# Kernel tuning notes

Hardware: AMD Instinct MI355X
Metric: run time of the kernel (lower is better)

## Reference

```python
import jax, jax.numpy as jnp
import numpy as np

DIM = 1024
NUM_HEADS = 16
HEAD_DIM = 64

def setup_inputs() -> dict:
    key = jax.random.key(0)
    ks = jax.random.split(key, 7)
    x = jax.random.normal(ks[0], (4, 4096, DIM), dtype=jnp.float32)
    mask = jnp.ones((4, 4096), dtype=jnp.float32)
    # torch Linear stores weight (out, in) and computes x @ W.T; we store (in, out) directly.
    Wq = jax.random.normal(ks[1], (DIM, NUM_HEADS * HEAD_DIM), dtype=jnp.float32) / np.sqrt(DIM)
    Wk = jax.random.normal(ks[2], (DIM, NUM_HEADS * HEAD_DIM), dtype=jnp.float32) / np.sqrt(DIM)
    Wv = jax.random.normal(ks[3], (DIM, NUM_HEADS * HEAD_DIM), dtype=jnp.float32) / np.sqrt(DIM)
    Wo = jax.random.normal(ks[4], (NUM_HEADS * HEAD_DIM, DIM), dtype=jnp.float32) / np.sqrt(NUM_HEADS * HEAD_DIM)
    # FeatureMap buffer: randn(dim, dim) / sqrt(dim) with dim = head_dim
    proj = jax.random.normal(ks[5], (HEAD_DIM, HEAD_DIM), dtype=jnp.float32) / np.sqrt(HEAD_DIM)
    return {"x": x, "mask": mask, "Wq": Wq, "Wk": Wk, "Wv": Wv, "Wo": Wo, "proj": proj}

def _feature_map(x, proj):
    # phi(x) = elu(x @ proj) + 1  (non-negative random features)
    return jax.nn.elu(x @ proj) + 1.0

def reference(x, mask, Wq, Wk, Wv, Wo, proj):
    b, n, _ = x.shape
    h, d = NUM_HEADS, HEAD_DIM
    # project and split heads: (b, h, n, d)
    q = (x @ Wq).reshape(b, n, h, d).transpose(0, 2, 1, 3)
    k = (x @ Wk).reshape(b, n, h, d).transpose(0, 2, 1, 3)
    v = (x @ Wv).reshape(b, n, h, d).transpose(0, 2, 1, 3)
    q = _feature_map(q, proj)
    k = _feature_map(k, proj)
    # mask: (b, n) -> (b, 1, n, 1)
    k = k * mask[:, None, :, None]
    # linear attention: phi(Q) (phi(K)^T V)
    kv = jnp.einsum('bhnd,bhne->bhde', k, v)          # (b, h, d, d)
    qkv = jnp.einsum('bhnd,bhde->bhne', q, kv)        # (b, h, n, d)
    k_sum = k.sum(axis=2)                              # (b, h, d)
    normalizer = jnp.einsum('bhnd,bhd->bhn', q, k_sum) + 1e-06
    out = qkv / normalizer[..., None]
    out = out.transpose(0, 2, 1, 3).reshape(b, n, h * d)
    return out @ Wo
```

## Files before the change

kernel.cpp:

```cpp
#include <hip/hip_runtime.h>
#include <stdint.h>

#define TOKENS 16384
#define KDIM 1024
#define QKVN 3072

typedef unsigned short u16;
using bf16x8 = __attribute__((ext_vector_type(8))) __bf16;
using f32x4  = __attribute__((ext_vector_type(4))) float;
using u16x8  = __attribute__((ext_vector_type(8))) unsigned short;

__device__ inline u16 f2bf(float f) {
  union { float f; uint32_t u; } v; v.f = f;
  uint32_t u = v.u;
  return (u16)((u + 0x7FFFu + ((u >> 16) & 1u)) >> 16);
}
__device__ inline float bf2f(u16 s) {
  union { uint32_t u; float f; } v; v.u = ((uint32_t)s) << 16;
  return v.f;
}
__device__ inline void g2l16(const void* g, void* l) {
  __builtin_amdgcn_global_load_lds(
      (const __attribute__((address_space(1))) void*)g,
      (__attribute__((address_space(3))) void*)l, 16, 0, 0);
}

template<int LD>
__device__ inline void stage_half(const u16* __restrict__ g, u16* l, int t) {
  #pragma unroll
  for (int i = 0; i < 2; ++i) {
    const int ch = i * 512 + t;
    const int row = ch >> 3;
    const int cc = (ch & 7) ^ (row & 7);
    g2l16(g + (long)row * LD + cc * 8, (char*)l + ch * 16);
  }
}

#define LDA_H(DST, BASE) do { \
  _Pragma("unroll") \
  for (int mi = 0; mi < 4; ++mi) { \
    const int row = wm*64 + mi*16 + rl; \
    const char* p = (const char*)(BASE) + row*128; \
    const int sw = (row & 7) << 4; \
    DST[mi][0] = *(const bf16x8*)(p + ((kg*16) ^ sw)); \
    DST[mi][1] = *(const bf16x8*)(p + ((64 + kg*16) ^ sw)); \
  } \
} while (0)

#define LDB_H(DST, BASE) do { \
  _Pragma("unroll") \
  for (int ni = 0; ni < 2; ++ni) { \
    const int row = wn*32 + ni*16 + rl; \
    const char* p = (const char*)(BASE) + row*128; \
    const int sw = (row & 7) << 4; \
    DST[ni][0] = *(const bf16x8*)(p + ((kg*16) ^ sw)); \
    DST[ni][1] = *(const bf16x8*)(p + ((64 + kg*16) ^ sw)); \
  } \
} while (0)

#define MFMAQ(MH, NH, AV, BV) do { \
  __builtin_amdgcn_s_setprio(1); \
  _Pragma("unroll") \
  for (int kh = 0; kh < 2; ++kh) \
    _Pragma("unroll") \
    for (int mi = 0; mi < 4; ++mi) \
      _Pragma("unroll") \
      for (int ni = 0; ni < 2; ++ni) \
        acc[(MH)*4+mi][(NH)*2+ni] = __builtin_amdgcn_mfma_f32_16x16x32_bf16( \
            AV[mi][kh], BV[ni][kh], acc[(MH)*4+mi][(NH)*2+ni], 0, 0, 0); \
  __builtin_amdgcn_s_setprio(0); \
} while (0)

#define LGKM0 do { \
  asm volatile("s_waitcnt lgkmcnt(0)" ::: "memory"); \
  __builtin_amdgcn_sched_barrier(0); \
} while (0)
#define LGKM_PRE(N) asm volatile("s_waitcnt lgkmcnt(" #N ")" ::: "memory")
#define VMC(N) asm volatile("s_waitcnt vmcnt(" #N ")" ::: "memory")
#define BAR() __builtin_amdgcn_s_barrier()

template<int NTOT, int EPI, int ALD, int NT, int PERB>
__global__ __launch_bounds__(512, 2) void gemm256(
    const u16* __restrict__ A, const u16* __restrict__ Bm,
    void* __restrict__ C, const float* __restrict__ aux) {
  __shared__ u16 As[2][2][8192];
  __shared__ u16 Bs[2][2][8192];
  const int t = threadIdx.x;
  const int l = t & 63;
  const int w = t >> 6;
  const int rl = l & 15, kg = l >> 4;
  const int wm = w >> 2, wn = w & 3;
  constexpr int nbn = NTOT / 256;
  constexpr int nwg = 64 * nbn;
  constexpr int GRID = nwg / NT;
  constexpr int KC = NT * 16;
  constexpr int IT = KC / 2;
  static_assert(nwg % 8 == 0, "bijective xcd swizzle");
  const int bid = blockIdx.x;

  auto tcoord = [&](int ot, long& tar, long& tbr) {
    const int gt = ot * GRID + bid;
    const int swz = (gt & 7) * (nwg / 8) + (gt >> 3);
    tar = (long)(swz / nbn) * 256;
    tbr = (long)(swz % nbn) * 256;
  };
  auto asrc = [&](int ch) {
    long ta, tb; tcoord(ch >> 4, ta, tb);
    return A + ta * ALD + (ch & 15) * 64;
  };
  auto bsrc = [&](int ch) {
    long ta, tb; tcoord(ch >> 4, ta, tb);
    return Bm + (PERB ? (ta >> 12) * 1048576 : 0) + tb * 1024 + (ch & 15) * 64;
  };

  f32x4 acc[8][4];
  #pragma unroll
  for (int i = 0; i < 8; ++i)
    #pragma unroll
    for (int j = 0; j < 4; ++j)
      acc[i][j] = (f32x4){0.f, 0.f, 0.f, 0.f};

  bf16x8 af[4][2], b0[2][2], b1[2][2];

  auto epilogue = [&](int ot) {
    long ar0, br0; tcoord(ot, ar0, br0);
    #pragma unroll
    for (int mh = 0; mh < 2; ++mh)
      #pragma unroll
      for (int mi = 0; mi < 4; ++mi)
        #pragma unroll
        for (int j = 0; j < 4; ++j) {
          const long row = ar0 + mh*128 + wm*64 + mi*16 + kg*4 + j;
          float rs = 0.f;
          if (EPI == 0) rs = aux[row];
          #pragma unroll
          for (int nh = 0; nh < 2; ++nh)
            #pragma unroll
            for (int ni = 0; ni < 2; ++ni) {
              const long col = br0 + nh*128 + wn*32 + ni*16 + rl;
              float v = acc[mh*4+mi][nh*2+ni][j];
              if (EPI == 0) {
                if (col < 2048) {
                  v = (v > 0.f) ? (v + 1.f) : __expf(v);
                  if (col >= 1024) v *= rs;
                }
                ((u16*)C)[row * QKVN + col] = f2bf(v);
              } else {
                ((float*)C)[row * NTOT + col] = v;
              }
            }
        }
    #pragma unroll
    for (int i = 0; i < 8; ++i)
      #pragma unroll
      for (int j = 0; j < 4; ++j)
        acc[i][j] = (f32x4){0.f, 0.f, 0.f, 0.f};
  };

  {
    const u16* A0s = asrc(0); const u16* B0s = bsrc(0);
    const u16* A1s = asrc(1); const u16* B1s = bsrc(1);
    stage_half<ALD >(A0s,             As[0][0], t);
    stage_half<1024>(B0s,             Bs[0][0], t);
    stage_half<1024>(B0s + 128*1024,  Bs[0][1], t);
    stage_half<ALD >(A0s + 128*ALD,   As[0][1], t);
    stage_half<ALD >(A1s,             As[1][0], t);
    stage_half<1024>(B1s,             Bs[1][0], t);
    stage_half<1024>(B1s + 128*1024,  Bs[1][1], t);
    VMC(6);
    BAR();
  }

  for (int i = 0; i < IT; ++i) {
    const int e = (2*i + 2 < KC) ? 2*i + 2 : KC - 1;
    const int o = (2*i + 3 < KC) ? 2*i + 3 : KC - 1;
    const u16* Ao1 = asrc(2*i + 1);
    const u16* Ae = asrc(e); const u16* Be = bsrc(e);
    const u16* Ao = asrc(o); const u16* Bo = bsrc(o);

    LDA_H(af, As[0][0]); LDB_H(b0, Bs[0][0]);
    stage_half<ALD>(Ao1 + 128*ALD, As[1][1], t);
    LGKM_PRE(8);
    BAR(); LGKM0;
    MFMAQ(0, 0, af, b0);
    BAR();
    LDB_H(b1, Bs[0][1]);
    stage_half<ALD>(Ae, As[0][0], t);
    BAR(); LGKM0;
    MFMAQ(0, 1, af, b1);
    BAR();
    LDA_H(af, As[0][1]);
    stage_half<1024>(Be, Bs[0][0], t);
    BAR(); LGKM0;
    MFMAQ(1, 0, af, b0);
    BAR();
    stage_half<1024>(Be + 128*1024, Bs[0][1], t);
    BAR();
    MFMAQ(1, 1, af, b1);
    VMC(6);
    BAR();
    LDA_H(af, As[1][0]); LDB_H(b0, Bs[1][0]);
    stage_half<ALD>(Ae + 128*ALD, As[0][1], t);
    LGKM_PRE(8);
    BAR(); LGKM0;
    MFMAQ(0, 0, af, b0);
    BAR();
    LDB_H(b1, Bs[1][1]);
    stage_half<ALD>(Ao, As[1][0], t);
    BAR(); LGKM0;
    MFMAQ(0, 1, af, b1);
    BAR();
    LDA_H(af, As[1][1]);
    stage_half<1024>(Bo, Bs[1][0], t);
    BAR(); LGKM0;
    MFMAQ(1, 0, af, b0);
    BAR();
    stage_half<1024>(Bo + 128*1024, Bs[1][1], t);
    BAR();
    MFMAQ(1, 1, af, b1);
    VMC(6);
    BAR();

    if ((i & 7) == 7) epilogue(i >> 3);
  }
  VMC(0);
}

__global__ __launch_bounds__(256) void kv_kernel(const u16* __restrict__ QKV,
    float* __restrict__ kvws, float* __restrict__ ksws) {
  __shared__ u16 Kl[32 * 64];
  __shared__ u16 Vl[32 * 64];
  const int t = threadIdx.x;
  const int l = t & 63, w = t >> 6;
  const int rl = l & 15, kg = l >> 4;
  const int bid = blockIdx.x;
  const int bh = bid >> 3, ns = bid & 7;
  const int b = bh >> 4, h = bh & 15;
  const long tok0 = (long)b * 4096 + ns * 512;

  f32x4 acc[4];
  #pragma unroll
  for (int i = 0; i < 4; ++i) acc[i] = (f32x4){0.f, 0.f, 0.f, 0.f};
  float ks = 0.f;
  const int srow = t >> 3, scc = t & 7;

  for (int it = 0; it < 16; ++it) {
    const long tb = tok0 + it * 32;
    g2l16(QKV + (tb + srow) * QKVN + 1024 + h * 64 + scc * 8, (char*)Kl + t * 16);
    g2l16(QKV + (tb + srow) * QKVN + 2048 + h * 64 + scc * 8, (char*)Vl + t * 16);
    __syncthreads();
    union { u16x8 u; bf16x8 v; } au, bu;
    #pragma unroll
    for (int j = 0; j < 8; ++j) au.u[j] = Kl[(kg * 8 + j) * 64 + w * 16 + rl];
    #pragma unroll
    for (int ni = 0; ni < 4; ++ni) {
      #pragma unroll
      for (int j = 0; j < 8; ++j) bu.u[j] = Vl[(kg * 8 + j) * 64 + ni * 16 + rl];
      acc[ni] = __builtin_amdgcn_mfma_f32_16x16x32_bf16(au.v, bu.v, acc[ni], 0, 0, 0);
    }
    #pragma unroll
    for (int r = 0; r < 8; ++r) ks += bf2f(Kl[(w * 8 + r) * 64 + (t & 63)]);
    __syncthreads();
  }
  float* kvb = kvws + bh * 4096;
  #pragma unroll
  for (int ni = 0; ni < 4; ++ni)
    #pragma unroll
    for (int j = 0; j < 4; ++j) {
      const int d = w * 16 + kg * 4 + j;
      const int e = ni * 16 + rl;
      atomicAdd(&kvb[d * 64 + e], acc[ni][j]);
    }
  atomicAdd(&ksws[bh * 64 + (t & 63)], ks);
}

__global__ __launch_bounds__(256) void scale_q(u16* __restrict__ QKV,
    const float* __restrict__ ksws) {
  __shared__ float ksl[1024];
  const int bid = blockIdx.x, t = threadIdx.x;
  const int n0 = bid * 16;
  const int b = n0 >> 12;
  #pragma unroll
  for (int i = 0; i < 4; ++i) ksl[i * 256 + t] = ksws[b * 1024 + i * 256 + t];
  __syncthreads();
  const int h = t & 15, ti = t >> 4;
  u16* qp = QKV + (long)(n0 + ti) * QKVN + h * 64;
  u16x8 v[8];
  float norm = 1e-6f;
  #pragma unroll
  for (int i = 0; i < 8; ++i) {
    v[i] = *(const u16x8*)(qp + i * 8);
    #pragma unroll
    for (int j = 0; j < 8; ++j) norm += bf2f(v[i][j]) * ksl[h * 64 + i * 8 + j];
  }
  const float inv = 1.0f / norm;
  #pragma unroll
  for (int i = 0; i < 8; ++i) {
    u16x8 o;
    #pragma unroll
    for (int j = 0; j < 8; ++j) o[j] = f2bf(bf2f(v[i][j]) * inv);
    *(u16x8*)(qp + i * 8) = o;
  }
}

__global__ __launch_bounds__(256) void w2_kernel(const float* __restrict__ kvws,
    const u16* __restrict__ WoT, u16* __restrict__ W2T) {
  __shared__ float kvl[64][64];
  const int bid = blockIdx.x, t = threadIdx.x;
  const int bh = bid >> 2, os = bid & 3;
  const int b = bh >> 4, h = bh & 15;
  const float* kvb = kvws + bh * 4096;
  #pragma unroll
  for (int i = 0; i < 16; ++i) ((float*)kvl)[i * 256 + t] = kvb[i * 256 + t];
  __syncthreads();
  const int o = os * 256 + t;
  float wo[64];
  const u16* wr = WoT + (long)o * 1024 + h * 64;
  #pragma unroll
  for (int i = 0; i < 8; ++i) {
    u16x8 v = *(const u16x8*)(wr + i * 8);
    #pragma unroll
    for (int j = 0; j < 8; ++j) wo[i * 8 + j] = bf2f(v[j]);
  }
  u16* out = W2T + (long)b * 1048576 + (long)o * 1024 + h * 64;
  for (int d = 0; d < 64; ++d) {
    float s = 0.f;
    #pragma unroll
    for (int e = 0; e < 64; ++e) s += wo[e] * kvl[d][e];
    out[d] = f2bf(s);
  }
}

__global__ __launch_bounds__(256) void prep_qk(const float* __restrict__ Wq,
    const float* __restrict__ Wk, const float* __restrict__ proj,
    u16* __restrict__ WqkvT) {
  __shared__ float Wl[128][65];
  __shared__ float Pl[64][65];
  const int bid = blockIdx.x;
  const int m = bid >> 7, h = (bid >> 3) & 15, cb = bid & 7;
  const float* W = m ? Wk : Wq;
  const int t = threadIdx.x;
  #pragma unroll
  for (int i = 0; i < 16; ++i) {
    const int idx = i * 256 + t;
    Pl[idx >> 6][idx & 63] = proj[idx];
  }
  #pragma unroll
  for (int i = 0; i < 32; ++i) {
    const int idx = i * 256 + t;
    const int c = idx >> 6, d = idx & 63;
    Wl[c][d] = W[(long)(cb * 128 + c) * 1024 + h * 64 + d];
  }
  __syncthreads();
  const int c = t & 127, j0 = (t >> 7) * 32;
  float a[32];
  #pragma unroll
  for (int jj = 0; jj < 32; ++jj) a[jj] = 0.f;
  for (int d = 0; d < 64; ++d) {
    const float wv = Wl[c][d];
    #pragma unroll
    for (int jj = 0; jj < 32; ++jj) a[jj] += wv * Pl[d][j0 + jj];
  }
  #pragma unroll
  for (int jj = 0; jj < 32; ++jj)
    WqkvT[(long)(m * 1024 + h * 64 + j0 + jj) * 1024 + cb * 128 + c] = f2bf(a[jj]);
}

__global__ __launch_bounds__(256) void prep_vo(const float* __restrict__ Wv,
    const float* __restrict__ Wo, u16* __restrict__ WqkvT, u16* __restrict__ WoT) {
  __shared__ float til[64][65];
  const int bid = blockIdx.x;
  const int which = bid >> 8, rt = (bid >> 4) & 15, ct = bid & 15;
  const float* S = which ? Wo : Wv;
  const int t = threadIdx.x;
  const int j = t & 63;
  #pragma unroll
  for (int p = 0; p < 16; ++p) {
    const int i = p * 4 + (t >> 6);
    til[i][j] = S[(long)(rt * 64 + i) * 1024 + ct * 64 + j];
  }
  __syncthreads();
  u16* dst = which ? WoT : (WqkvT + (long)2048 * 1024);
  #pragma unroll
  for (int p = 0; p < 16; ++p) {
    const int i = p * 4 + (t >> 6);
    dst[(long)(ct * 64 + i) * 1024 + rt * 64 + j] = f2bf(til[j][i]);
  }
}

__global__ __launch_bounds__(256) void conv_x(const float* __restrict__ x,
                                              u16* __restrict__ xb) {
  const int idx = blockIdx.x * 256 + threadIdx.x;
  const float4* p = (const float4*)x + (long)idx * 2;
  const float4 a = p[0], b = p[1];
  u16x8 o;
  o[0] = f2bf(a.x); o[1] = f2bf(a.y); o[2] = f2bf(a.z); o[3] = f2bf(a.w);
  o[4] = f2bf(b.x); o[5] = f2bf(b.y); o[6] = f2bf(b.z); o[7] = f2bf(b.w);
  *((u16x8*)xb + idx) = o;
}

extern "C" void kernel_launch(void* const* d_in, const int* in_sizes, int n_in,
                              void* d_out, int out_size, void* d_ws, size_t ws_size,
                              hipStream_t stream) {
  const float* x    = (const float*)d_in[0];
  const float* mask = (const float*)d_in[1];
  const float* Wq   = (const float*)d_in[2];
  const float* Wk   = (const float*)d_in[3];
  const float* Wv   = (const float*)d_in[4];
  const float* Wo   = (const float*)d_in[5];
  const float* proj = (const float*)d_in[6];

  char* ws = (char*)d_ws;
  u16*  WqkvT = (u16*)(ws);
  u16*  WoT   = (u16*)(ws + 6291456);
  u16*  xb    = (u16*)(ws + 8388608);
  u16*  QKV   = (u16*)(ws + 41943040);
  float* kvws = (float*)(ws + 142606336);
  float* ksws = (float*)(ws + 143654912);
  u16*  W2T  = (u16*)(ws + 8388608);
  if (ws_size < (size_t)143671296) return;

  hipMemsetAsync(kvws, 0, 1064960, stream);
  prep_qk<<<256, 256, 0, stream>>>(Wq, Wk, proj, WqkvT);
  prep_vo<<<512, 256, 0, stream>>>(Wv, Wo, WqkvT, WoT);
  conv_x <<<8192, 256, 0, stream>>>(x, xb);
  gemm256<3072, 0, 1024, 3, 0><<<256, 512, 0, stream>>>(xb, WqkvT, (void*)QKV, mask);
  kv_kernel<<<512, 256, 0, stream>>>(QKV, kvws, ksws);
  scale_q<<<1024, 256, 0, stream>>>((u16*)QKV, ksws);
  w2_kernel<<<256, 256, 0, stream>>>(kvws, WoT, W2T);
  gemm256<1024, 1, 3072, 1, 1><<<256, 512, 0, stream>>>(QKV, W2T, d_out, nullptr);
}
```

Measured before the change: 277.1 us.

## Double-buffer register fragments and drop explicit LDS waits in GEMM main loop

```diff
diff --git a/kernel.cpp b/kernel.cpp
--- a/kernel.cpp
+++ b/kernel.cpp
@@ -71,13 +71,9 @@
   __builtin_amdgcn_s_setprio(0); \
 } while (0)
 
-#define LGKM0 do { \
-  asm volatile("s_waitcnt lgkmcnt(0)" ::: "memory"); \
-  __builtin_amdgcn_sched_barrier(0); \
-} while (0)
-#define LGKM_PRE(N) asm volatile("s_waitcnt lgkmcnt(" #N ")" ::: "memory")
 #define VMC(N) asm volatile("s_waitcnt vmcnt(" #N ")" ::: "memory")
 #define BAR() __builtin_amdgcn_s_barrier()
+#define SCHED0 __builtin_amdgcn_sched_barrier(0)
 
 template<int NTOT, int EPI, int ALD, int NT, int PERB>
 __global__ __launch_bounds__(512, 2) void gemm256(
@@ -120,7 +116,7 @@
     for (int j = 0; j < 4; ++j)
       acc[i][j] = (f32x4){0.f, 0.f, 0.f, 0.f};
 
-  bf16x8 af[4][2], b0[2][2], b1[2][2];
+  bf16x8 afA[4][2], afB[4][2], bA[2][2], bB[2][2];
 
   auto epilogue = [&](int ot) {
     long ar0, br0; tcoord(ot, ar0, br0);
@@ -167,8 +163,10 @@
     stage_half<ALD >(A1s,             As[1][0], t);
     stage_half<1024>(B1s,             Bs[1][0], t);
     stage_half<1024>(B1s + 128*1024,  Bs[1][1], t);
-    VMC(6);
+    VMC(8);
     BAR();
+    LDA_H(afA, As[0][0]);
+    LDB_H(bA, Bs[0][0]);
   }
 
   for (int i = 0; i < IT; ++i) {
@@ -178,48 +176,46 @@
     const u16* Ae = asrc(e); const u16* Be = bsrc(e);
     const u16* Ao = asrc(o); const u16* Bo = bsrc(o);
 
-    LDA_H(af, As[0][0]); LDB_H(b0, Bs[0][0]);
+    LDB_H(bB, Bs[0][1]);
     stage_half<ALD>(Ao1 + 128*ALD, As[1][1], t);
-    LGKM_PRE(8);
-    BAR(); LGKM0;
-    MFMAQ(0, 0, af, b0);
-    BAR();
-    LDB_H(b1, Bs[0][1]);
+    SCHED0;
+    MFMAQ(0, 0, afA, bA);
+    SCHED0; VMC(8); BAR();
+    LDA_H(afB, As[0][1]);
     stage_half<ALD>(Ae, As[0][0], t);
-    BAR(); LGKM0;
-    MFMAQ(0, 1, af, b1);
-    BAR();
-    LDA_H(af, As[0][1]);
+    SCHED0;
+    MFMAQ(0, 1, afA, bB);
+    SCHED0; VMC(8); BAR();
+    LDA_H(afA, As[1][0]);
     stage_half<1024>(Be, Bs[0][0], t);
-    BAR(); LGKM0;
-    MFMAQ(1, 0, af, b0);
-    BAR();
+    SCHED0;
+    MFMAQ(1, 0, afB, bA);
+    SCHED0; VMC(8); BAR();
+    LDB_H(bA, Bs[1][0]);
     stage_half<1024>(Be + 128*1024, Bs[0][1], t);
-    BAR();
-    MFMAQ(1, 1, af, b1);
-    VMC(6);
-    BAR();
-    LDA_H(af, As[1][0]); LDB_H(b0, Bs[1][0]);
+    SCHED0;
+    MFMAQ(1, 1, afB, bB);
+    SCHED0; VMC(8); BAR();
+    LDB_H(bB, Bs[1][1]);
     stage_half<ALD>(Ae + 128*ALD, As[0][1], t);
-    LGKM_PRE(8);
-    BAR(); LGKM0;
-    MFMAQ(0, 0, af, b0);
-    BAR();
-    LDB_H(b1, Bs[1][1]);
+    SCHED0;
+    MFMAQ(0, 0, afA, bA);
+    SCHED0; VMC(8); BAR();
+    LDA_H(afB, As[1][1]);
     stage_half<ALD>(Ao, As[1][0], t);
-    BAR(); LGKM0;
-    MFMAQ(0, 1, af, b1);
-    BAR();
-    LDA_H(af, As[1][1]);
+    SCHED0;
+    MFMAQ(0, 1, afA, bB);
+    SCHED0; VMC(8); BAR();
+    LDA_H(afA, As[0][0]);
     stage_half<1024>(Bo, Bs[1][0], t);
-    BAR(); LGKM0;
-    MFMAQ(1, 0, af, b0);
-    BAR();
+    SCHED0;
+    MFMAQ(1, 0, afB, bA);
+    SCHED0; VMC(8); BAR();
+    LDB_H(bA, Bs[0][0]);
     stage_half<1024>(Bo + 128*1024, Bs[1][1], t);
-    BAR();
-    MFMAQ(1, 1, af, b1);
-    VMC(6);
-    BAR();
+    SCHED0;
+    MFMAQ(1, 1, afB, bB);
+    SCHED0; VMC(8); BAR();
 
     if ((i & 7) == 7) epilogue(i >> 3);
   }
```

After: 291.4 us. 5.2% more time.
